# Performance work log

Measured on AMD Instinct MI355X. Metric: run time of the kernel, lower is better.

The kernel has to match this reference:

```python
import jax, jax.numpy as jnp
import numpy as np

Q_MIN, Q_MAX = -128.0, 127.0  # int8 range (brevitas signed, narrow_range=False)


def ste_round(x):
    # straight-through round (matches brevitas training semantics)
    return x + jax.lax.stop_gradient(jnp.round(x) - x)


def fake_quant(x, s):
    # per-tensor int8 quant-dequant: clamp(round(x/s), -128, 127) * s
    return jnp.clip(ste_round(x / s), Q_MIN, Q_MAX) * s


def conv2d(x, w):
    # NCHW x OIHW, stride 1, VALID padding (kernel (3,3), no padding arg in source)
    return jax.lax.conv_general_dilated(
        x, w, window_strides=(1, 1), padding='VALID',
        dimension_numbers=('NCHW', 'OIHW', 'NCHW'))


def setup_inputs() -> dict:
    key = jax.random.key(0)
    k = jax.random.split(key, 5)
    x = jax.random.normal(k[0], (32, 5, 512, 512), jnp.float32)
    w1 = jax.random.normal(k[1], (10, 5, 3, 3), jnp.float32) * 0.1
    b1 = jax.random.normal(k[2], (10,), jnp.float32) * 0.1
    w2 = jax.random.normal(k[3], (10, 10, 3, 3), jnp.float32) * 0.1
    b2 = jax.random.normal(k[4], (10,), jnp.float32) * 0.1
    # fixed-point (power-of-two) per-tensor scales
    s_in = jnp.full((1,), 2.0 ** -4, jnp.float32)
    s_w1 = jnp.full((1,), 2.0 ** -7, jnp.float32)
    s_o1 = jnp.full((1,), 2.0 ** -4, jnp.float32)
    s_w2 = jnp.full((1,), 2.0 ** -7, jnp.float32)
    s_o2 = jnp.full((1,), 2.0 ** -4, jnp.float32)
    return {"x": x, "w1": w1, "b1": b1, "w2": w2, "b2": b2,
            "s_in": s_in, "s_w1": s_w1, "s_o1": s_o1, "s_w2": s_w2, "s_o2": s_o2}


def reference(x, w1, b1, w2, b2, s_in, s_w1, s_o1, s_w2, s_o2):
    # QuantIdentity(Int8ActPerTensorFixedPoint)
    xq = fake_quant(x, s_in)
    # QuantConv2d #1: weight quant, bias quant (scale = in_scale*w_scale), output quant
    w1q = fake_quant(w1, s_w1)
    b1q = fake_quant(b1, s_in * s_w1)
    y = conv2d(xq, w1q) + b1q[None, :, None, None]  # [32,10,510,510]
    yq = fake_quant(y, s_o1)
    # QuantConv2d #2
    w2q = fake_quant(w2, s_w2)
    b2q = fake_quant(b2, s_o1 * s_w2)
    z = conv2d(yq, w2q) + b2q[None, :, None, None]  # [32,10,508,508]
    return fake_quant(z, s_o2)
```

## Files before the change

kernel.cpp:

```cpp
#include <hip/hip_runtime.h>


#define XQ_OFF   8192
#define YQ_OFF   41951488ULL

__device__ __forceinline__ float qclamp(float v) {
    return fminf(fmaxf(v, -128.0f), 127.0f);
}

__device__ __forceinline__ int dot4(int a, int b, int c) {
#if __has_builtin(__builtin_amdgcn_sdot4)
    return __builtin_amdgcn_sdot4(a, b, c, false);
#else
    c += ((a << 24) >> 24) * ((b << 24) >> 24);
    c += ((a << 16) >> 24) * ((b << 16) >> 24);
    c += ((a <<  8) >> 24) * ((b <<  8) >> 24);
    c += (a >> 24) * (b >> 24);
    return c;
#endif
}

__device__ __forceinline__ int alignb(int hi, int lo, int sh) {
#if __has_builtin(__builtin_amdgcn_alignbyte)
    return __builtin_amdgcn_alignbyte(hi, lo, sh);
#else
    return (int)((((unsigned long long)(unsigned)hi << 32) | (unsigned)lo) >> (8 * sh));
#endif
}

__global__ __launch_bounds__(256) void prep_kernel(
    const float* __restrict__ w1, const float* __restrict__ b1,
    const float* __restrict__ w2, const float* __restrict__ b2,
    const float* __restrict__ s_in, const float* __restrict__ s_w1,
    const float* __restrict__ s_o1, const float* __restrict__ s_w2,
    const float* __restrict__ s_o2,
    float* __restrict__ consts, int* __restrict__ wp1, int* __restrict__ b1i,
    int* __restrict__ wp2, int* __restrict__ b2i)
{
    int t = threadIdx.x;
    float si = s_in[0], sw1 = s_w1[0], so1 = s_o1[0], sw2 = s_w2[0], so2 = s_o2[0];
    if (t == 0) {
        consts[0] = 1.0f / si;
        consts[1] = (si * sw1) / so1;
        consts[2] = (so1 * sw2) / so2;
        consts[3] = so2;
    }
    for (int i = t; i < 150; i += 256) {
        int oc = i / 15, rem = i % 15, c = rem / 3, kh = rem % 3;
        const float* src = w1 + (((oc * 5 + c) * 3 + kh) * 3);
        int q0 = (int)qclamp(rintf(src[0] / sw1));
        int q1 = (int)qclamp(rintf(src[1] / sw1));
        int q2 = (int)qclamp(rintf(src[2] / sw1));
        wp1[(c * 3 + kh) * 10 + oc] = (q0 & 255) | ((q1 & 255) << 8) | ((q2 & 255) << 16);
    }
    for (int i = t; i < 10; i += 256)
        b1i[i] = (int)qclamp(rintf(b1[i] / (si * sw1)));
    for (int i = t; i < 300; i += 256) {
        int oc = i / 30, rem = i % 30, c = rem / 3, kh = rem % 3;
        const float* src = w2 + (((oc * 10 + c) * 3 + kh) * 3);
        int q0 = (int)qclamp(rintf(src[0] / sw2));
        int q1 = (int)qclamp(rintf(src[1] / sw2));
        int q2 = (int)qclamp(rintf(src[2] / sw2));
        wp2[(c * 3 + kh) * 10 + oc] = (q0 & 255) | ((q1 & 255) << 8) | ((q2 & 255) << 16);
    }
    for (int i = t; i < 10; i += 256)
        b2i[i] = (int)qclamp(rintf(b2[i] / (so1 * sw2)));
}

__global__ __launch_bounds__(256) void quant_x_kernel(
    const float4* __restrict__ x, const float* __restrict__ consts,
    int* __restrict__ xq, int n4)
{
    int i = blockIdx.x * 256 + threadIdx.x;
    if (i >= n4) return;
    float inv = consts[0];
    float4 v = x[i];
    int q0 = (int)qclamp(rintf(v.x * inv));
    int q1 = (int)qclamp(rintf(v.y * inv));
    int q2 = (int)qclamp(rintf(v.z * inv));
    int q3 = (int)qclamp(rintf(v.w * inv));
    xq[i] = (q0 & 255) | ((q1 & 255) << 8) | ((q2 & 255) << 16) | (q3 << 24);
}

__global__ __launch_bounds__(256) void conv1_kernel(
    const signed char* __restrict__ xq, const int* __restrict__ wp,
    const int* __restrict__ bi, const float* __restrict__ consts,
    signed char* __restrict__ yq)
{
    int t = blockIdx.x * 256 + threadIdx.x;
    int owt = t & 127;
    int r = t >> 7;
    int oh = r % 510;
    int n = r / 510;
    int ow0 = owt << 2;

    int acc[10][4];
    #pragma unroll
    for (int oc = 0; oc < 10; ++oc) {
        int b = bi[oc];
        acc[oc][0] = b; acc[oc][1] = b; acc[oc][2] = b; acc[oc][3] = b;
    }

    const signed char* xb = xq + (size_t)n * (5 * 512 * 512) + oh * 512 + ow0;
    #pragma unroll
    for (int c = 0; c < 5; ++c) {
        #pragma unroll
        for (int kh = 0; kh < 3; ++kh) {
            const int* pi = (const int*)(xb + c * 262144 + kh * 512);
            int u0 = pi[0];
            int u1 = pi[1];
            int win0 = u0;
            int win1 = alignb(u1, u0, 1);
            int win2 = alignb(u1, u0, 2);
            int win3 = alignb(u1, u0, 3);
            const int* wrow = wp + (c * 3 + kh) * 10;
            #pragma unroll
            for (int oc = 0; oc < 10; ++oc) {
                int w = wrow[oc];
                acc[oc][0] = dot4(win0, w, acc[oc][0]);
                acc[oc][1] = dot4(win1, w, acc[oc][1]);
                acc[oc][2] = dot4(win2, w, acc[oc][2]);
                acc[oc][3] = dot4(win3, w, acc[oc][3]);
            }
        }
    }

    float cr1 = consts[1];
    if (owt < 127) {
        #pragma unroll
        for (int oc = 0; oc < 10; ++oc) {
            int q0 = (int)qclamp(rintf((float)acc[oc][0] * cr1));
            int q1 = (int)qclamp(rintf((float)acc[oc][1] * cr1));
            int q2 = (int)qclamp(rintf((float)acc[oc][2] * cr1));
            int q3 = (int)qclamp(rintf((float)acc[oc][3] * cr1));
            size_t idx = (((size_t)(n * 10 + oc) * 510) + oh) * 512 + ow0;
            *(int*)(yq + idx) = (q0 & 255) | ((q1 & 255) << 8) |
                                ((q2 & 255) << 16) | (q3 << 24);
        }
    } else {
        #pragma unroll
        for (int oc = 0; oc < 10; ++oc) {
            size_t idx = (((size_t)(n * 10 + oc) * 510) + oh) * 512 + ow0;
            yq[idx + 0] = (signed char)(int)qclamp(rintf((float)acc[oc][0] * cr1));
            yq[idx + 1] = (signed char)(int)qclamp(rintf((float)acc[oc][1] * cr1));
        }
    }
}

__global__ __launch_bounds__(256) void conv2_kernel(
    const signed char* __restrict__ yq, const int* __restrict__ wp,
    const int* __restrict__ bi, const float* __restrict__ consts,
    float* __restrict__ out)
{
    int t = blockIdx.x * 256 + threadIdx.x;
    int owt = t % 127;
    int r = t / 127;
    int oh = r % 508;
    int n = r / 508;
    if (n >= 32) return;
    int ow0 = owt << 2;

    int acc[10][4];
    #pragma unroll
    for (int oc = 0; oc < 10; ++oc) {
        int b = bi[oc];
        acc[oc][0] = b; acc[oc][1] = b; acc[oc][2] = b; acc[oc][3] = b;
    }

    const signed char* yb = yq + (size_t)n * (10 * 510 * 512) + (size_t)oh * 512 + ow0;
    #pragma unroll
    for (int c = 0; c < 10; ++c) {
        #pragma unroll
        for (int kh = 0; kh < 3; ++kh) {
            const int* pi = (const int*)(yb + (size_t)c * (510 * 512) + kh * 512);
            int u0 = pi[0];
            int u1 = pi[1];
            int win0 = u0;
            int win1 = alignb(u1, u0, 1);
            int win2 = alignb(u1, u0, 2);
            int win3 = alignb(u1, u0, 3);
            const int* wrow = wp + (c * 3 + kh) * 10;
            #pragma unroll
            for (int oc = 0; oc < 10; ++oc) {
                int w = wrow[oc];
                acc[oc][0] = dot4(win0, w, acc[oc][0]);
                acc[oc][1] = dot4(win1, w, acc[oc][1]);
                acc[oc][2] = dot4(win2, w, acc[oc][2]);
                acc[oc][3] = dot4(win3, w, acc[oc][3]);
            }
        }
    }

    float cr2 = consts[2];
    float so = consts[3];
    #pragma unroll
    for (int oc = 0; oc < 10; ++oc) {
        float4 v;
        v.x = qclamp(rintf((float)acc[oc][0] * cr2)) * so;
        v.y = qclamp(rintf((float)acc[oc][1] * cr2)) * so;
        v.z = qclamp(rintf((float)acc[oc][2] * cr2)) * so;
        v.w = qclamp(rintf((float)acc[oc][3] * cr2)) * so;
        size_t idx = (((size_t)(n * 10 + oc) * 508) + oh) * 508 + ow0;
        *(float4*)(out + idx) = v;
    }
}

extern "C" void kernel_launch(void* const* d_in, const int* in_sizes, int n_in,
                              void* d_out, int out_size, void* d_ws, size_t ws_size,
                              hipStream_t stream) {
    const float* x    = (const float*)d_in[0];
    const float* w1   = (const float*)d_in[1];
    const float* b1   = (const float*)d_in[2];
    const float* w2   = (const float*)d_in[3];
    const float* b2   = (const float*)d_in[4];
    const float* s_in = (const float*)d_in[5];
    const float* s_w1 = (const float*)d_in[6];
    const float* s_o1 = (const float*)d_in[7];
    const float* s_w2 = (const float*)d_in[8];
    const float* s_o2 = (const float*)d_in[9];

    char* ws = (char*)d_ws;
    float* consts = (float*)ws;
    int* wp1 = (int*)(ws + 256);
    int* b1i = (int*)(ws + 1280);
    int* wp2 = (int*)(ws + 2048);
    int* b2i = (int*)(ws + 3584);
    signed char* xqb = (signed char*)(ws + XQ_OFF);
    signed char* yqb = (signed char*)(ws + YQ_OFF);

    prep_kernel<<<1, 256, 0, stream>>>(w1, b1, w2, b2, s_in, s_w1, s_o1, s_w2, s_o2,
                                       consts, wp1, b1i, wp2, b2i);

    int n4 = 32 * 5 * 512 * 512 / 4;
    quant_x_kernel<<<(n4 + 255) / 256, 256, 0, stream>>>(
        (const float4*)x, consts, (int*)xqb, n4);

    conv1_kernel<<<8160, 256, 0, stream>>>(xqb, wp1, b1i, consts, yqb);

    conv2_kernel<<<8065, 256, 0, stream>>>(yqb, wp2, b2i, consts, (float*)d_out);
}
```

Before: 583.8 us.

## Rewrite both quantized convolutions as int8 MFMA implicit GEMMs

Replaces the per-thread sdot4 convolution loops with wavefront-level int8 MFMA (16x16x64) implicit GEMMs. Weights are repacked in the prep kernel into the MFMA A-operand layout, and each wave walks down output rows building the B operand from shifted input bytes. This is meant to cut the heavy VALU dot-product cost. In exchange, outputs are written as scalar per-lane stores instead of vectorized ones, and each lane issues many small redundant loads.

```diff
diff --git a/kernel.cpp b/kernel.cpp
--- a/kernel.cpp
+++ b/kernel.cpp
@@ -4,20 +4,10 @@
 #define XQ_OFF   8192
 #define YQ_OFF   41951488ULL
 
+typedef int v4i __attribute__((ext_vector_type(4)));
+
 __device__ __forceinline__ float qclamp(float v) {
     return fminf(fmaxf(v, -128.0f), 127.0f);
-}
-
-__device__ __forceinline__ int dot4(int a, int b, int c) {
-#if __has_builtin(__builtin_amdgcn_sdot4)
-    return __builtin_amdgcn_sdot4(a, b, c, false);
-#else
-    c += ((a << 24) >> 24) * ((b << 24) >> 24);
-    c += ((a << 16) >> 24) * ((b << 16) >> 24);
-    c += ((a <<  8) >> 24) * ((b <<  8) >> 24);
-    c += (a >> 24) * (b >> 24);
-    return c;
-#endif
 }
 
 __device__ __forceinline__ int alignb(int hi, int lo, int sh) {
@@ -34,8 +24,8 @@
     const float* __restrict__ s_in, const float* __restrict__ s_w1,
     const float* __restrict__ s_o1, const float* __restrict__ s_w2,
     const float* __restrict__ s_o2,
-    float* __restrict__ consts, int* __restrict__ wp1, int* __restrict__ b1i,
-    int* __restrict__ wp2, int* __restrict__ b2i)
+    float* __restrict__ consts, int* __restrict__ wA1, int* __restrict__ b1i,
+    int* __restrict__ wA2, int* __restrict__ b2i)
 {
     int t = threadIdx.x;
     float si = s_in[0], sw1 = s_w1[0], so1 = s_o1[0], sw2 = s_w2[0], so2 = s_o2[0];
@@ -45,26 +35,41 @@
         consts[2] = (so1 * sw2) / so2;
         consts[3] = so2;
     }
-    for (int i = t; i < 150; i += 256) {
-        int oc = i / 15, rem = i % 15, c = rem / 3, kh = rem % 3;
-        const float* src = w1 + (((oc * 5 + c) * 3 + kh) * 3);
-        int q0 = (int)qclamp(rintf(src[0] / sw1));
-        int q1 = (int)qclamp(rintf(src[1] / sw1));
-        int q2 = (int)qclamp(rintf(src[2] / sw1));
-        wp1[(c * 3 + kh) * 10 + oc] = (q0 & 255) | ((q1 & 255) << 8) | ((q2 & 255) << 16);
-    }
-    for (int i = t; i < 10; i += 256)
-        b1i[i] = (int)qclamp(rintf(b1[i] / (si * sw1)));
-    for (int i = t; i < 300; i += 256) {
-        int oc = i / 30, rem = i % 30, c = rem / 3, kh = rem % 3;
-        const float* src = w2 + (((oc * 10 + c) * 3 + kh) * 3);
-        int q0 = (int)qclamp(rintf(src[0] / sw2));
-        int q1 = (int)qclamp(rintf(src[1] / sw2));
-        int q2 = (int)qclamp(rintf(src[2] / sw2));
-        wp2[(c * 3 + kh) * 10 + oc] = (q0 & 255) | ((q1 & 255) << 8) | ((q2 & 255) << 16);
-    }
-    for (int i = t; i < 10; i += 256)
-        b2i[i] = (int)qclamp(rintf(b2[i] / (so1 * sw2)));
+    {
+        int l = t >> 2, r = t & 3;
+        int g = l >> 4, m = l & 15;
+        int d = 4 * g + r;
+        int val = 0;
+        if (d < 15 && m < 10) {
+            int c = d / 3, kh = d % 3;
+            const float* src = w1 + (((m * 5 + c) * 3 + kh) * 3);
+            int q0 = (int)qclamp(rintf(src[0] / sw1));
+            int q1 = (int)qclamp(rintf(src[1] / sw1));
+            int q2 = (int)qclamp(rintf(src[2] / sw1));
+            val = (q0 & 255) | ((q1 & 255) << 8) | ((q2 & 255) << 16);
+        }
+        wA1[t] = val;
+    }
+    for (int i = t; i < 512; i += 256) {
+        int l = i >> 3, r = i & 7;
+        int g = l >> 4, m = l & 15;
+        int f = r >> 2;
+        int d = f * 16 + 4 * g + (r & 3);
+        int val = 0;
+        if (d < 30 && m < 10) {
+            int c = d / 3, kh = d % 3;
+            const float* src = w2 + (((m * 10 + c) * 3 + kh) * 3);
+            int q0 = (int)qclamp(rintf(src[0] / sw2));
+            int q1 = (int)qclamp(rintf(src[1] / sw2));
+            int q2 = (int)qclamp(rintf(src[2] / sw2));
+            val = (q0 & 255) | ((q1 & 255) << 8) | ((q2 & 255) << 16);
+        }
+        wA2[i] = val;
+    }
+    if (t < 16) {
+        b1i[t] = (t < 10) ? (int)qclamp(rintf(b1[t] / (si * sw1))) : 0;
+        b2i[t] = (t < 10) ? (int)qclamp(rintf(b2[t] / (so1 * sw2))) : 0;
+    }
 }
 
 __global__ __launch_bounds__(256) void quant_x_kernel(
@@ -82,126 +87,123 @@
     xq[i] = (q0 & 255) | ((q1 & 255) << 8) | ((q2 & 255) << 16) | (q3 << 24);
 }
 
-__global__ __launch_bounds__(256) void conv1_kernel(
-    const signed char* __restrict__ xq, const int* __restrict__ wp,
+__global__ __launch_bounds__(256) void conv1_mfma(
+    const signed char* __restrict__ xq, const int* __restrict__ wA,
     const int* __restrict__ bi, const float* __restrict__ consts,
     signed char* __restrict__ yq)
 {
-    int t = blockIdx.x * 256 + threadIdx.x;
-    int owt = t & 127;
-    int r = t >> 7;
-    int oh = r % 510;
-    int n = r / 510;
-    int ow0 = owt << 2;
-
-    int acc[10][4];
-    #pragma unroll
-    for (int oc = 0; oc < 10; ++oc) {
-        int b = bi[oc];
-        acc[oc][0] = b; acc[oc][1] = b; acc[oc][2] = b; acc[oc][3] = b;
-    }
-
-    const signed char* xb = xq + (size_t)n * (5 * 512 * 512) + oh * 512 + ow0;
-    #pragma unroll
-    for (int c = 0; c < 5; ++c) {
-        #pragma unroll
-        for (int kh = 0; kh < 3; ++kh) {
-            const int* pi = (const int*)(xb + c * 262144 + kh * 512);
-            int u0 = pi[0];
-            int u1 = pi[1];
-            int win0 = u0;
-            int win1 = alignb(u1, u0, 1);
-            int win2 = alignb(u1, u0, 2);
-            int win3 = alignb(u1, u0, 3);
-            const int* wrow = wp + (c * 3 + kh) * 10;
-            #pragma unroll
-            for (int oc = 0; oc < 10; ++oc) {
-                int w = wrow[oc];
-                acc[oc][0] = dot4(win0, w, acc[oc][0]);
-                acc[oc][1] = dot4(win1, w, acc[oc][1]);
-                acc[oc][2] = dot4(win2, w, acc[oc][2]);
-                acc[oc][3] = dot4(win3, w, acc[oc][3]);
+    int lane = threadIdx.x & 63;
+    int W = blockIdx.x * 4 + (threadIdx.x >> 6);
+    int owt = W & 31;
+    int rem = W >> 5;
+    int ohc = rem % 17;
+    int n = rem / 17;
+    int g = lane >> 4, m = lane & 15;
+    int ow0 = owt << 4;
+
+    v4i a = ((const v4i*)wA)[lane];
+    v4i cinit;
+    #pragma unroll
+    for (int r = 0; r < 4; ++r) cinit[r] = bi[4 * g + r];
+
+    int koff[4];
+    #pragma unroll
+    for (int s = 0; s < 4; ++s) {
+        int d = 4 * g + s;
+        koff[s] = (d < 15) ? (d / 3) * 262144 + (d % 3) * 512 : 0;
+    }
+    int xoff = ow0 + (m & ~3);
+    int sh = m & 3;
+    int oh0 = ohc * 30;
+    int base = n * (5 * 512 * 512) + oh0 * 512 + xoff;
+    float cr1 = consts[1];
+    bool owv = (ow0 + m) < 510;
+    size_t sbase = (((size_t)(n * 10) * 510) + oh0) * 512 + ow0 + m;
+
+    for (int i = 0; i < 30; ++i) {
+        v4i b;
+        #pragma unroll
+        for (int s = 0; s < 4; ++s) {
+            const int* p = (const int*)(xq + base + koff[s]);
+            int u0 = p[0], u1 = p[1];
+            b[s] = alignb(u1, u0, sh);
+        }
+        v4i acc = __builtin_amdgcn_mfma_i32_16x16x64_i8(a, b, cinit, 0, 0, 0);
+        #pragma unroll
+        for (int r = 0; r < 4; ++r) {
+            int oc = 4 * g + r;
+            if (oc < 10 && owv) {
+                int q = (int)qclamp(rintf((float)acc[r] * cr1));
+                yq[sbase + (size_t)oc * (510 * 512)] = (signed char)q;
             }
         }
-    }
-
-    float cr1 = consts[1];
-    if (owt < 127) {
-        #pragma unroll
-        for (int oc = 0; oc < 10; ++oc) {
-            int q0 = (int)qclamp(rintf((float)acc[oc][0] * cr1));
-            int q1 = (int)qclamp(rintf((float)acc[oc][1] * cr1));
-            int q2 = (int)qclamp(rintf((float)acc[oc][2] * cr1));
-            int q3 = (int)qclamp(rintf((float)acc[oc][3] * cr1));
-            size_t idx = (((size_t)(n * 10 + oc) * 510) + oh) * 512 + ow0;
-            *(int*)(yq + idx) = (q0 & 255) | ((q1 & 255) << 8) |
-                                ((q2 & 255) << 16) | (q3 << 24);
-        }
-    } else {
-        #pragma unroll
-        for (int oc = 0; oc < 10; ++oc) {
-            size_t idx = (((size_t)(n * 10 + oc) * 510) + oh) * 512 + ow0;
-            yq[idx + 0] = (signed char)(int)qclamp(rintf((float)acc[oc][0] * cr1));
-            yq[idx + 1] = (signed char)(int)qclamp(rintf((float)acc[oc][1] * cr1));
-        }
-    }
-}
-
-__global__ __launch_bounds__(256) void conv2_kernel(
-    const signed char* __restrict__ yq, const int* __restrict__ wp,
+        base += 512;
+        sbase += 512;
+    }
+}
+
+__global__ __launch_bounds__(256) void conv2_mfma(
+    const signed char* __restrict__ yq, const int* __restrict__ wA,
     const int* __restrict__ bi, const float* __restrict__ consts,
     float* __restrict__ out)
 {
-    int t = blockIdx.x * 256 + threadIdx.x;
-    int owt = t % 127;
-    int r = t / 127;
-    int oh = r % 508;
-    int n = r / 508;
-    if (n >= 32) return;
-    int ow0 = owt << 2;
-
-    int acc[10][4];
-    #pragma unroll
-    for (int oc = 0; oc < 10; ++oc) {
-        int b = bi[oc];
-        acc[oc][0] = b; acc[oc][1] = b; acc[oc][2] = b; acc[oc][3] = b;
-    }
-
-    const signed char* yb = yq + (size_t)n * (10 * 510 * 512) + (size_t)oh * 512 + ow0;
-    #pragma unroll
-    for (int c = 0; c < 10; ++c) {
-        #pragma unroll
-        for (int kh = 0; kh < 3; ++kh) {
-            const int* pi = (const int*)(yb + (size_t)c * (510 * 512) + kh * 512);
-            int u0 = pi[0];
-            int u1 = pi[1];
-            int win0 = u0;
-            int win1 = alignb(u1, u0, 1);
-            int win2 = alignb(u1, u0, 2);
-            int win3 = alignb(u1, u0, 3);
-            const int* wrow = wp + (c * 3 + kh) * 10;
-            #pragma unroll
-            for (int oc = 0; oc < 10; ++oc) {
-                int w = wrow[oc];
-                acc[oc][0] = dot4(win0, w, acc[oc][0]);
-                acc[oc][1] = dot4(win1, w, acc[oc][1]);
-                acc[oc][2] = dot4(win2, w, acc[oc][2]);
-                acc[oc][3] = dot4(win3, w, acc[oc][3]);
+    int lane = threadIdx.x & 63;
+    int W = blockIdx.x * 4 + (threadIdx.x >> 6);
+    int owt = W & 31;
+    int ohc = (W >> 5) & 15;
+    int n = W >> 9;
+    int g = lane >> 4, m = lane & 15;
+    int ow0 = owt << 4;
+
+    const v4i* wA4 = (const v4i*)wA;
+    v4i a0 = wA4[lane * 2 + 0];
+    v4i a1 = wA4[lane * 2 + 1];
+    v4i cinit;
+    #pragma unroll
+    for (int r = 0; r < 4; ++r) cinit[r] = bi[4 * g + r];
+
+    int koff[8];
+    #pragma unroll
+    for (int s = 0; s < 8; ++s) {
+        int d = (s >> 2) * 16 + 4 * g + (s & 3);
+        koff[s] = (d < 30) ? (d / 3) * (510 * 512) + (d % 3) * 512 : 0;
+    }
+    int xoff = ow0 + (m & ~3);
+    int sh = m & 3;
+    int oh0 = ohc * 32;
+    int base = n * (10 * 510 * 512) + oh0 * 512 + xoff;
+    float cr2 = consts[2];
+    float so  = consts[3];
+    bool owv = (ow0 + m) < 508;
+    size_t sbase = (((size_t)(n * 10) * 508) + oh0) * 508 + ow0 + m;
+    int iters = (508 - oh0 < 32) ? (508 - oh0) : 32;
+
+    for (int i = 0; i < iters; ++i) {
+        v4i b0, b1v;
+        #pragma unroll
+        for (int s = 0; s < 4; ++s) {
+            const int* p = (const int*)(yq + base + koff[s]);
+            int u0 = p[0], u1 = p[1];
+            b0[s] = alignb(u1, u0, sh);
+        }
+        #pragma unroll
+        for (int s = 4; s < 8; ++s) {
+            const int* p = (const int*)(yq + base + koff[s]);
+            int u0 = p[0], u1 = p[1];
+            b1v[s - 4] = alignb(u1, u0, sh);
+        }
+        v4i acc = __builtin_amdgcn_mfma_i32_16x16x64_i8(a0, b0, cinit, 0, 0, 0);
+        acc = __builtin_amdgcn_mfma_i32_16x16x64_i8(a1, b1v, acc, 0, 0, 0);
+        #pragma unroll
+        for (int r = 0; r < 4; ++r) {
+            int oc = 4 * g + r;
+            if (oc < 10 && owv) {
+                float v = qclamp(rintf((float)acc[r] * cr2)) * so;
+                out[sbase + (size_t)oc * (508 * 508)] = v;
             }
         }
-    }
-
-    float cr2 = consts[2];
-    float so = consts[3];
-    #pragma unroll
-    for (int oc = 0; oc < 10; ++oc) {
-        float4 v;
-        v.x = qclamp(rintf((float)acc[oc][0] * cr2)) * so;
-        v.y = qclamp(rintf((float)acc[oc][1] * cr2)) * so;
-        v.z = qclamp(rintf((float)acc[oc][2] * cr2)) * so;
-        v.w = qclamp(rintf((float)acc[oc][3] * cr2)) * so;
-        size_t idx = (((size_t)(n * 10 + oc) * 508) + oh) * 508 + ow0;
-        *(float4*)(out + idx) = v;
+        base += 512;
+        sbase += 508;
     }
 }
 
@@ -221,21 +223,21 @@
 
     char* ws = (char*)d_ws;
     float* consts = (float*)ws;
-    int* wp1 = (int*)(ws + 256);
+    int* wA1 = (int*)(ws + 256);
     int* b1i = (int*)(ws + 1280);
-    int* wp2 = (int*)(ws + 2048);
-    int* b2i = (int*)(ws + 3584);
+    int* wA2 = (int*)(ws + 2048);
+    int* b2i = (int*)(ws + 4096);
     signed char* xqb = (signed char*)(ws + XQ_OFF);
     signed char* yqb = (signed char*)(ws + YQ_OFF);
 
     prep_kernel<<<1, 256, 0, stream>>>(w1, b1, w2, b2, s_in, s_w1, s_o1, s_w2, s_o2,
-                                       consts, wp1, b1i, wp2, b2i);
+                                       consts, wA1, b1i, wA2, b2i);
 
     int n4 = 32 * 5 * 512 * 512 / 4;
     quant_x_kernel<<<(n4 + 255) / 256, 256, 0, stream>>>(
         (const float4*)x, consts, (int*)xqb, n4);
 
-    conv1_kernel<<<8160, 256, 0, stream>>>(xqb, wp1, b1i, consts, yqb);
-
-    conv2_kernel<<<8065, 256, 0, stream>>>(yqb, wp2, b2i, consts, (float*)d_out);
-}
+    conv1_mfma<<<4352, 256, 0, stream>>>(xqb, wA1, b1i, consts, yqb);
+
+    conv2_mfma<<<4096, 256, 0, stream>>>(yqb, wA2, b2i, consts, (float*)d_out);
+}
```

Measured after the change: 703.9 us. +20.6%, slower.
